# Kernel optimization log

Hardware: AMD Instinct MI355X
Metric: run time of the kernel (lower is better)

## Reference

```python
import jax, jax.numpy as jnp
import numpy as np

B, S, HID = 1, 4096, 2048
NH, NKV, HD = 16, 4, 128
BLK, LOCAL, GLOB, STRIDE = 128, 4, 4, 8
NEG = -1e9


def _rotate_half(x):
    x1 = x[..., : x.shape[-1] // 2]
    x2 = x[..., x.shape[-1] // 2 :]
    return jnp.concatenate([-x2, x1], axis=-1)


def setup_inputs() -> dict:
    key = jax.random.key(0)
    ks = jax.random.split(key, 6)
    hidden_states = jax.random.normal(ks[0], (B, S, HID), jnp.float32)
    attention_mask_2d = jnp.ones((B, S), jnp.float32)
    # RoPE tables (b=1 broadcasts over batch, heads)
    pos = jnp.arange(S, dtype=jnp.float32)
    inv = 1.0 / (10000.0 ** (jnp.arange(0, HD, 2, dtype=jnp.float32) / HD))
    fr = pos[:, None] * inv[None, :]
    emb = jnp.concatenate([fr, fr], axis=-1)
    cos = jnp.cos(emb)[None]
    sin = jnp.sin(emb)[None]
    sc = 0.02
    Wq = jax.random.normal(ks[1], (HID, NH * HD), jnp.float32) * sc
    Wk = jax.random.normal(ks[2], (HID, NKV * HD), jnp.float32) * sc
    Wv = jax.random.normal(ks[3], (HID, NKV * HD), jnp.float32) * sc
    Wo = jax.random.normal(ks[4], (NH * HD, HID), jnp.float32) * sc
    return dict(hidden_states=hidden_states, attention_mask_2d=attention_mask_2d,
                cos=cos, sin=sin, Wq=Wq, Wk=Wk, Wv=Wv, Wo=Wo)


def reference(hidden_states, attention_mask_2d, cos, sin, Wq, Wk, Wv, Wo):
    b, Sq, _ = hidden_states.shape
    q = (hidden_states @ Wq).reshape(b, Sq, NH, HD).transpose(0, 2, 1, 3)
    k = (hidden_states @ Wk).reshape(b, Sq, NKV, HD).transpose(0, 2, 1, 3)
    v = (hidden_states @ Wv).reshape(b, Sq, NKV, HD).transpose(0, 2, 1, 3)
    c, s = cos[:, None], sin[:, None]  # broadcast over heads
    q = q * c + _rotate_half(q) * s
    k = k * c + _rotate_half(k) * s
    rep = NH // NKV
    k = jnp.repeat(k, rep, axis=1)
    v = jnp.repeat(v, rep, axis=1)

    scaling = HD ** -0.5
    N = Sq // BLK  # seq divisible by block_size -> pad=0 in the original
    qb = q.reshape(b, NH, N, BLK, HD).astype(jnp.float32)
    kb = k.reshape(b, NH, N, BLK, HD).astype(jnp.float32)
    vb = v.reshape(b, NH, N, BLK, HD).astype(jnp.float32)
    km = attention_mask_2d.reshape(b, N, BLK)

    # ---- local windows: LOCAL blocks ending at the current block ----
    Lp = LOCAL - 1
    kp = jnp.pad(kb, ((0, 0), (0, 0), (Lp, 0), (0, 0), (0, 0)))
    vp = jnp.pad(vb, ((0, 0), (0, 0), (Lp, 0), (0, 0), (0, 0)))
    kmp = jnp.pad(km, ((0, 0), (Lp, 0), (0, 0)))  # padded blocks masked (0)
    win = jnp.arange(N)[:, None] + jnp.arange(LOCAL)[None, :]  # (N, LOCAL)
    k_local = kp[:, :, win]          # (b,h,N,LOCAL,BLK,HD)
    v_local = vp[:, :, win]
    km_local = kmp[:, win]           # (b,N,LOCAL,BLK)

    s_local = jnp.einsum('bhntd,bhnlsd->bhntls', qb, k_local) * scaling
    s_local = s_local + (1.0 - km_local)[:, None, :, None, :, :] * NEG
    intra = jnp.triu(jnp.full((BLK, BLK), NEG, jnp.float32), 1)  # causal inside current block only
    s_local = s_local.at[:, :, :, :, -1, :].add(intra)
    s_local = s_local.reshape(b, NH, N, BLK, LOCAL * BLK)

    # ---- global blocks: block 0 + strided past blocks, dedup -> masked ----
    i = jnp.arange(N)
    offsets = jnp.arange(GLOB - 1, 0, -1) * STRIDE
    idx = jnp.clip(i[:, None] - offsets[None, :], 0)
    idx = jnp.concatenate([jnp.zeros((N, 1), idx.dtype), idx], axis=1)  # (N, GLOB)
    dup = idx[:, 1:] == idx[:, :-1]
    g_valid = jnp.concatenate([jnp.ones((N, 1), bool), ~dup], axis=1).astype(jnp.float32)
    k_g = kb[:, :, idx]              # (b,h,N,GLOB,BLK,HD) gather of global blocks
    v_g = vb[:, :, idx]
    km_g = km[:, idx] * g_valid[None, :, :, None]  # (b,N,GLOB,BLK)

    s_g = jnp.einsum('bhntd,bhngsd->bhntgs', qb, k_g) * scaling
    s_g = s_g + (1.0 - km_g)[:, None, :, None, :, :] * NEG
    s_g = s_g.reshape(b, NH, N, BLK, GLOB * BLK)

    scores = jnp.concatenate([s_local, s_g], axis=-1)  # (b,h,N,BLK,(LOCAL+GLOB)*BLK)
    v_all = jnp.concatenate([v_local.reshape(b, NH, N, LOCAL * BLK, HD),
                             v_g.reshape(b, NH, N, GLOB * BLK, HD)], axis=-2)
    probs = jax.nn.softmax(scores, axis=-1)  # dropout_p = 0 (eval)
    out = jnp.einsum('bhntk,bhnkd->bhntd', probs, v_all)
    out = out.reshape(b, NH, Sq, HD).transpose(0, 2, 1, 3).reshape(b, Sq, NH * HD)
    return out @ Wo
```

## Files before the change

kernel.cpp:

```cpp
#include <hip/hip_runtime.h>
#include <hip/hip_bf16.h>
#include <cstdint>

#define NEGV   (-1000000000.0f)
#define SCALE  0.08838834764831845f
#define LOG2E  1.4426950408889634f
#define QSC    (SCALE * LOG2E)
#define NEGL2  (NEGV * LOG2E)

typedef __bf16 bf16x8 __attribute__((ext_vector_type(8)));
typedef float  f32x4  __attribute__((ext_vector_type(4)));
typedef unsigned short u16;
typedef unsigned int   u32;

#define MFMA16(a, b, c) __builtin_amdgcn_mfma_f32_16x16x32_bf16((a), (b), (c), 0, 0, 0)

#define WS_XP    ((size_t)0)
#define WS_AOP   ((size_t)0)
#define WS_WQP   ((size_t)8388608)
#define WS_WKP   ((size_t)12582912)
#define WS_WVP   ((size_t)13631488)
#define WS_WOP   ((size_t)14680064)
#define WS_QF    ((size_t)18874368)
#define WS_KF    ((size_t)27262976)
#define WS_VF    ((size_t)29360128)

__device__ __forceinline__ u16 f2bf(float f) {
  union { float f; u32 u; } v; v.f = f;
  u32 u = v.u;
  u += 0x7FFFu + ((u >> 16) & 1u);
  return (u16)(u >> 16);
}

__device__ __forceinline__ void gl_lds16(const u16* g, u16* l) {
  __builtin_amdgcn_global_load_lds((const __attribute__((address_space(1))) u32*)g,
                                   (__attribute__((address_space(3))) u32*)l,
                                   16, 0, 0);
}

__device__ __forceinline__ int fragoff(int row, int k) {
  return ((row >> 4) * 64 + ((k >> 3) & 3) * 16 + (row & 15)) * 8 + (k & 7);
}

__global__ __launch_bounds__(256, 4)
void convert_kernel(const float* __restrict__ X,
                    const float* __restrict__ Wq,
                    const float* __restrict__ Wk,
                    const float* __restrict__ Wv,
                    const float* __restrict__ Wo,
                    u16* __restrict__ ws)
{
  const int t = blockIdx.x;
  const int tid = threadIdx.x;
  const float* src; u16* dst; int tt, ldn; bool amode = false;
  if (t < 2048)      { src = X;  dst = ws + WS_XP;  tt = t;        ldn = 2048; amode = true; }
  else if (t < 3072) { src = Wq; dst = ws + WS_WQP; tt = t - 2048; ldn = 2048; }
  else if (t < 3328) { src = Wk; dst = ws + WS_WKP; tt = t - 3072; ldn = 512;  }
  else if (t < 3584) { src = Wv; dst = ws + WS_WVP; tt = t - 3328; ldn = 512;  }
  else               { src = Wo; dst = ws + WS_WOP; tt = t - 3584; ldn = 2048; }
  const int rb = tt >> 6, kb = tt & 63;

  if (amode) {
    #pragma unroll
    for (int p = 0; p < 2; ++p) {
      const int c = tid + 256 * p;
      const int row = (c >> 6) * 16 + (c & 15);
      const int k0  = ((c >> 4) & 3) * 8;
      union { u16 h[8]; uint4 v; } pk;
      const float* s0 = src + (size_t)(rb * 128 + row) * 2048 + kb * 32 + k0;
      const float4 a0 = *reinterpret_cast<const float4*>(s0);
      const float4 a1 = *reinterpret_cast<const float4*>(s0 + 4);
      pk.h[0] = f2bf(a0.x); pk.h[1] = f2bf(a0.y); pk.h[2] = f2bf(a0.z); pk.h[3] = f2bf(a0.w);
      pk.h[4] = f2bf(a1.x); pk.h[5] = f2bf(a1.y); pk.h[6] = f2bf(a1.z); pk.h[7] = f2bf(a1.w);
      *reinterpret_cast<uint4*>(dst + (size_t)tt * 4096 + c * 8) = pk.v;
    }
  } else {
    __shared__ u16 Ls[32][136];
    #pragma unroll
    for (int i = 0; i < 4; ++i) {
      const int c = tid + 256 * i;
      const int k = c >> 5, n4 = c & 31;
      const float4 wv = *reinterpret_cast<const float4*>(
          src + (size_t)(kb * 32 + k) * ldn + rb * 128 + n4 * 4);
      u16* d = &Ls[k][n4 * 4];
      d[0] = f2bf(wv.x); d[1] = f2bf(wv.y); d[2] = f2bf(wv.z); d[3] = f2bf(wv.w);
    }
    __syncthreads();
    #pragma unroll
    for (int p = 0; p < 2; ++p) {
      const int c = tid + 256 * p;
      const int row = (c >> 6) * 16 + (c & 15);
      const int k0  = ((c >> 4) & 3) * 8;
      union { u16 h[8]; uint4 v; } pk;
      #pragma unroll
      for (int j = 0; j < 8; ++j) pk.h[j] = Ls[k0 + j][row];
      *reinterpret_cast<uint4*>(dst + (size_t)tt * 4096 + c * 8) = pk.v;
    }
  }
}

__device__ __forceinline__ void gemm_core(const u16* __restrict__ pa,
                                          const u16* __restrict__ pb,
                                          u16* As, u16* Bs,
                                          int tid, int wave, int lane,
                                          f32x4 acc[2][8])
{
  for (int it = 0; it < 64; ++it) {
    __syncthreads();
    gl_lds16(pa + tid * 8,         As + tid * 8);
    gl_lds16(pa + (tid + 256) * 8, As + (tid + 256) * 8);
    gl_lds16(pb + tid * 8,         Bs + tid * 8);
    gl_lds16(pb + (tid + 256) * 8, Bs + (tid + 256) * 8);
    pa += 4096; pb += 4096;
    __syncthreads();
    bf16x8 af0 = *reinterpret_cast<const bf16x8*>(As + (wave * 2 + 0) * 512 + lane * 8);
    bf16x8 af1 = *reinterpret_cast<const bf16x8*>(As + (wave * 2 + 1) * 512 + lane * 8);
    #pragma unroll
    for (int nt = 0; nt < 8; ++nt) {
      const bf16x8 bfr = *reinterpret_cast<const bf16x8*>(Bs + nt * 512 + lane * 8);
      acc[0][nt] = MFMA16(af0, bfr, acc[0][nt]);
      acc[1][nt] = MFMA16(af1, bfr, acc[1][nt]);
    }
  }
}

__global__ __launch_bounds__(256, 2)
void qkv_kernel(const float* __restrict__ cosp,
                const float* __restrict__ sinp,
                u16* __restrict__ ws)
{
  const int mb = blockIdx.x, bn = blockIdx.y;
  const int tid = threadIdx.x;
  const int wave = tid >> 6, lane = tid & 63;
  const int lq = lane >> 4, l16 = lane & 15;

  const u16* Ab = ws + WS_XP + (size_t)mb * 64 * 4096;
  const u16* Bb; int seg, hh;
  if (bn < 16)      { Bb = ws + WS_WQP + (size_t)bn * 64 * 4096;        seg = 0; hh = bn; }
  else if (bn < 20) { Bb = ws + WS_WKP + (size_t)(bn - 16) * 64 * 4096; seg = 1; hh = bn - 16; }
  else              { Bb = ws + WS_WVP + (size_t)(bn - 20) * 64 * 4096; seg = 2; hh = bn - 20; }

  __shared__ __align__(16) u16 As[4096];
  __shared__ __align__(16) u16 Bs[4096];

  f32x4 acc[2][8];
  #pragma unroll
  for (int i = 0; i < 2; ++i)
    #pragma unroll
    for (int j = 0; j < 8; ++j)
      #pragma unroll
      for (int r = 0; r < 4; ++r) acc[i][j][r] = 0.0f;

  gemm_core(Ab, Bb, As, Bs, tid, wave, lane, acc);

  const int m0 = mb * 128;
  if (seg == 2) {
    u16* V = ws + WS_VF + (size_t)hh * 524288;
    #pragma unroll
    for (int mt = 0; mt < 2; ++mt)
      #pragma unroll
      for (int nt = 0; nt < 8; ++nt) {
        const int d = nt * 16 + l16;
        #pragma unroll
        for (int r = 0; r < 4; ++r) {
          const int s = m0 + wave * 32 + mt * 16 + lq * 4 + r;
          V[(s >> 5) * 4096 + fragoff(d, s & 31)] = f2bf(acc[mt][nt][r]);
        }
      }
  } else {
    u16* D = ws + ((seg == 0) ? WS_QF : WS_KF) + (size_t)hh * 524288;
    const float qs = (seg == 0) ? QSC : 1.0f;
    #pragma unroll
    for (int mt = 0; mt < 2; ++mt)
      #pragma unroll
      for (int r = 0; r < 4; ++r) {
        const int s = m0 + wave * 32 + mt * 16 + lq * 4 + r;
        const int sl = s & 127;
        u16* Dt = D + (size_t)(s >> 7) * 16384;
        #pragma unroll
        for (int nt = 0; nt < 4; ++nt) {
          const int d1 = nt * 16 + l16, d2 = d1 + 64;
          const float c  = cosp[s * 128 + d1];
          const float sn = sinp[s * 128 + d1];
          const float v1 = acc[mt][nt][r], v2 = acc[mt][nt + 4][r];
          Dt[(d1 >> 5) * 4096 + fragoff(sl, d1 & 31)] = f2bf((v1 * c - v2 * sn) * qs);
          Dt[(d2 >> 5) * 4096 + fragoff(sl, d2 & 31)] = f2bf((v2 * c + v1 * sn) * qs);
        }
      }
  }
}

__global__ __launch_bounds__(512, 2)
void attn_kernel(const float* __restrict__ amask, u16* __restrict__ ws)
{
  extern __shared__ u16 smem[];
  u16* bufK = smem;
  u16* bufV = smem + 16384;
  const int bx = blockIdx.x;
  const int n = 31 - (bx >> 4);
  const int h = bx & 15;
  const int kvh = h >> 2;
  const int tid = threadIdx.x;
  const int wave = tid >> 6, lane = tid & 63;
  const int lq = lane >> 4, l16 = lane & 15;

  const u16* Kfb = ws + WS_KF + (size_t)kvh * 524288;
  const u16* Vfb = ws + WS_VF + (size_t)kvh * 524288;
  u16* AOp = ws + WS_AOP;
  u16* Pw = smem + 32768 + wave * 2048;

  const u16* Qb = ws + WS_QF + (size_t)h * 524288 + (size_t)n * 16384;
  bf16x8 qf[4];
  #pragma unroll
  for (int kk = 0; kk < 4; ++kk)
    qf[kk] = *reinterpret_cast<const bf16x8*>(Qb + (size_t)kk * 4096 + (wave * 64 + lane) * 8);

  f32x4 O[8];
  #pragma unroll
  for (int j = 0; j < 8; ++j)
    #pragma unroll
    for (int r = 0; r < 4; ++r) O[j][r] = 0.0f;
  float mrow[4], lrow[4];
  #pragma unroll
  for (int r = 0; r < 4; ++r) { mrow[r] = -3.0e38f; lrow[r] = 0.0f; }

  const int L = (n < 3 ? n : 3) + 1;
  const int G = (n >= 25) ? 3 : (n >= 17) ? 2 : (n >= 9) ? 1 : 0;
  const int nv = L + 1 + G;
  #define KBOF(i) ((i) < L ? n - L + 1 + (i) : ((i) == L ? 0 : n - 8 * (G - ((i) - L - 1))))

  uint4 pk[4], pv[4]; float biasN[8];
  {
    const int b0 = KBOF(0);
    const u16* Kb = Kfb + (size_t)b0 * 16384;
    const u16* Vb = Vfb + (size_t)b0 * 16384;
    #pragma unroll
    for (int p = 0; p < 4; ++p) {
      pk[p] = *reinterpret_cast<const uint4*>(Kb + (tid + 512 * p) * 8);
      pv[p] = *reinterpret_cast<const uint4*>(Vb + (tid + 512 * p) * 8);
    }
    #pragma unroll
    for (int nt = 0; nt < 8; ++nt)
      biasN[nt] = (1.0f - amask[b0 * 128 + nt * 16 + l16]) * NEGL2;
  }

  #pragma unroll
  for (int i = 0; i < 8; ++i) {
    if (i >= nv) break;
    const bool intra = (i == L - 1);

    __syncthreads();
    #pragma unroll
    for (int p = 0; p < 4; ++p) {
      *reinterpret_cast<uint4*>(bufK + (tid + 512 * p) * 8) = pk[p];
      *reinterpret_cast<uint4*>(bufV + (tid + 512 * p) * 8) = pv[p];
    }
    float biasC[8];
    #pragma unroll
    for (int nt = 0; nt < 8; ++nt) biasC[nt] = biasN[nt];
    if (i + 1 < nv) {
      const int nb = KBOF(i + 1);
      const u16* Kb = Kfb + (size_t)nb * 16384;
      const u16* Vb = Vfb + (size_t)nb * 16384;
      #pragma unroll
      for (int p = 0; p < 4; ++p) {
        pk[p] = *reinterpret_cast<const uint4*>(Kb + (tid + 512 * p) * 8);
        pv[p] = *reinterpret_cast<const uint4*>(Vb + (tid + 512 * p) * 8);
      }
      #pragma unroll
      for (int nt = 0; nt < 8; ++nt)
        biasN[nt] = (1.0f - amask[nb * 128 + nt * 16 + l16]) * NEGL2;
    }
    __syncthreads();

    f32x4 sacc[8];
    #pragma unroll
    for (int j = 0; j < 8; ++j)
      #pragma unroll
      for (int r = 0; r < 4; ++r) sacc[j][r] = 0.0f;
    #pragma unroll
    for (int kk = 0; kk < 4; ++kk)
      #pragma unroll
      for (int nt = 0; nt < 8; ++nt) {
        const bf16x8 bfr = *reinterpret_cast<const bf16x8*>(
            bufK + ((kk * 8 + nt) * 64 + lane) * 8);
        sacc[nt] = MFMA16(qf[kk], bfr, sacc[nt]);
      }

    #pragma unroll
    for (int r = 0; r < 4; ++r) {
      const int tq = wave * 16 + lq * 4 + r;
      float sv[8];
      float rmax = -3.0e38f;
      #pragma unroll
      for (int nt = 0; nt < 8; ++nt) {
        float s = sacc[nt][r] + biasC[nt];
        const int tk = nt * 16 + l16;
        if (intra && tk > tq) s += NEGL2;
        sv[nt] = s;
        rmax = fmaxf(rmax, s);
      }
      #pragma unroll
      for (int off = 1; off < 16; off <<= 1)
        rmax = fmaxf(rmax, __shfl_xor(rmax, off, 64));
      const float mold = mrow[r];
      const float mnew = fmaxf(mold, rmax);
      const float alpha = exp2f(mold - mnew);
      float rsum = 0.0f;
      u16 pb[8];
      #pragma unroll
      for (int nt = 0; nt < 8; ++nt) {
        const float pe = exp2f(sv[nt] - mnew);
        rsum += pe;
        pb[nt] = f2bf(pe);
      }
      #pragma unroll
      for (int off = 1; off < 16; off <<= 1)
        rsum += __shfl_xor(rsum, off, 64);
      lrow[r] = lrow[r] * alpha + rsum;
      mrow[r] = mnew;
      #pragma unroll
      for (int nt = 0; nt < 8; ++nt) O[nt][r] *= alpha;
      #pragma unroll
      for (int nt = 0; nt < 8; ++nt)
        Pw[(nt >> 1) * 512 + ((((nt & 1) * 2 + (l16 >> 3)) * 16) + lq * 4 + r) * 8 + (l16 & 7)] = pb[nt];
    }

    #pragma unroll
    for (int kk = 0; kk < 4; ++kk) {
      const bf16x8 pf = *reinterpret_cast<const bf16x8*>(Pw + kk * 512 + lane * 8);
      #pragma unroll
      for (int nt = 0; nt < 8; ++nt) {
        const bf16x8 vfr = *reinterpret_cast<const bf16x8*>(
            bufV + ((kk * 8 + nt) * 64 + lane) * 8);
        O[nt] = MFMA16(pf, vfr, O[nt]);
      }
    }
  }
  #undef KBOF

  #pragma unroll
  for (int r = 0; r < 4; ++r) {
    const float inv = 1.0f / lrow[r];
    const int s = n * 128 + wave * 16 + lq * 4 + r;
    #pragma unroll
    for (int nt = 0; nt < 8; ++nt) {
      const int kcol = h * 128 + nt * 16 + l16;
      AOp[((size_t)(s >> 7) * 64 + (kcol >> 5)) * 4096 + fragoff(s & 127, kcol & 31)] =
          f2bf(O[nt][r] * inv);
    }
  }
}

__global__ __launch_bounds__(256, 2)
void outproj_kernel(const u16* __restrict__ ws, float* __restrict__ Out)
{
  const int mb = blockIdx.x, bn = blockIdx.y;
  const int tid = threadIdx.x;
  const int wave = tid >> 6, lane = tid & 63;
  const int lq = lane >> 4, l16 = lane & 15;

  const u16* Ab = ws + WS_AOP + (size_t)mb * 64 * 4096;
  const u16* Bb = ws + WS_WOP + (size_t)bn * 64 * 4096;

  __shared__ __align__(16) u16 As[4096];
  __shared__ __align__(16) u16 Bs[4096];

  f32x4 acc[2][8];
  #pragma unroll
  for (int i = 0; i < 2; ++i)
    #pragma unroll
    for (int j = 0; j < 8; ++j)
      #pragma unroll
      for (int r = 0; r < 4; ++r) acc[i][j][r] = 0.0f;

  gemm_core(Ab, Bb, (u16*)As, (u16*)Bs, tid, wave, lane, acc);

  #pragma unroll
  for (int mt = 0; mt < 2; ++mt)
    #pragma unroll
    for (int nt = 0; nt < 8; ++nt) {
      const int ccol = bn * 128 + nt * 16 + l16;
      #pragma unroll
      for (int r = 0; r < 4; ++r) {
        const int s = mb * 128 + wave * 32 + mt * 16 + lq * 4 + r;
        Out[(size_t)s * 2048 + ccol] = acc[mt][nt][r];
      }
    }
}

extern "C" void kernel_launch(void* const* d_in, const int* in_sizes, int n_in,
                              void* d_out, int out_size, void* d_ws, size_t ws_size,
                              hipStream_t stream) {
  const float* X     = (const float*)d_in[0];
  const float* amask = (const float*)d_in[1];
  const float* cosp  = (const float*)d_in[2];
  const float* sinp  = (const float*)d_in[3];
  const float* Wq    = (const float*)d_in[4];
  const float* Wk    = (const float*)d_in[5];
  const float* Wv    = (const float*)d_in[6];
  const float* Wo    = (const float*)d_in[7];
  float* Out = (float*)d_out;
  u16* ws = (u16*)d_ws;

  static int lds_set = 0;
  (void)hipFuncSetAttribute((const void*)attn_kernel,
                            hipFuncAttributeMaxDynamicSharedMemorySize, 98304);
  (void)lds_set;

  hipLaunchKernelGGL(convert_kernel, dim3(4608), dim3(256), 0, stream,
                     X, Wq, Wk, Wv, Wo, ws);
  hipLaunchKernelGGL(qkv_kernel, dim3(32, 24), dim3(256), 0, stream,
                     cosp, sinp, ws);
  hipLaunchKernelGGL(attn_kernel, dim3(512), dim3(512), 98304, stream,
                     amask, ws);
  hipLaunchKernelGGL(outproj_kernel, dim3(32, 16), dim3(256), 0, stream,
                     ws, Out);
}
```

Before: 345.5 us.

## Share K/V tiles across two heads per block with async double-buffered LDS loads

The attention kernel now has each 512-thread block handle two query heads of the same KV group, each wave covering 32 query rows, so every K/V tile staged in LDS serves twice as many MFMAs. Register-staged prefetch is replaced with direct global-to-LDS loads into a double buffer, removing a barrier per iteration and the register copy. The intent is to halve redundant K/V loads and overlap loading with compute. In exchange it uses 144KB of LDS and more registers per block, which limits occupancy, launches 256 blocks instead of 512, and drops the reversed block order that gave load balancing. Launch bounds for the two GEMM kernels are also raised to 3 blocks per CU.

```diff
diff --git a/kernel.cpp b/kernel.cpp
--- a/kernel.cpp
+++ b/kernel.cpp
@@ -124,7 +124,7 @@
   }
 }
 
-__global__ __launch_bounds__(256, 2)
+__global__ __launch_bounds__(256, 3)
 void qkv_kernel(const float* __restrict__ cosp,
                 const float* __restrict__ sinp,
                 u16* __restrict__ ws)
@@ -193,166 +193,180 @@
 __global__ __launch_bounds__(512, 2)
 void attn_kernel(const float* __restrict__ amask, u16* __restrict__ ws)
 {
-  extern __shared__ u16 smem[];
-  u16* bufK = smem;
-  u16* bufV = smem + 16384;
-  const int bx = blockIdx.x;
-  const int n = 31 - (bx >> 4);
-  const int h = bx & 15;
-  const int kvh = h >> 2;
+  extern __shared__ __align__(16) u16 smem[];
+  const int bx  = blockIdx.x;
+  const int n   = bx >> 3;
+  const int sub = bx & 7;
+  const int kvh = sub >> 1;
   const int tid = threadIdx.x;
   const int wave = tid >> 6, lane = tid & 63;
   const int lq = lane >> 4, l16 = lane & 15;
+  const int h = kvh * 4 + (sub & 1) * 2 + (wave >> 2);
+  const int wq = wave & 3;
 
   const u16* Kfb = ws + WS_KF + (size_t)kvh * 524288;
   const u16* Vfb = ws + WS_VF + (size_t)kvh * 524288;
   u16* AOp = ws + WS_AOP;
-  u16* Pw = smem + 32768 + wave * 2048;
+  u16* Pw = smem + 65536 + wave * 1024;
 
   const u16* Qb = ws + WS_QF + (size_t)h * 524288 + (size_t)n * 16384;
-  bf16x8 qf[4];
-  #pragma unroll
-  for (int kk = 0; kk < 4; ++kk)
-    qf[kk] = *reinterpret_cast<const bf16x8*>(Qb + (size_t)kk * 4096 + (wave * 64 + lane) * 8);
-
-  f32x4 O[8];
-  #pragma unroll
-  for (int j = 0; j < 8; ++j)
-    #pragma unroll
-    for (int r = 0; r < 4; ++r) O[j][r] = 0.0f;
-  float mrow[4], lrow[4];
-  #pragma unroll
-  for (int r = 0; r < 4; ++r) { mrow[r] = -3.0e38f; lrow[r] = 0.0f; }
+  bf16x8 qf[2][4];
+  #pragma unroll
+  for (int mt = 0; mt < 2; ++mt)
+    #pragma unroll
+    for (int kk = 0; kk < 4; ++kk)
+      qf[mt][kk] = *reinterpret_cast<const bf16x8*>(
+          Qb + (size_t)kk * 4096 + ((wq * 2 + mt) * 64 + lane) * 8);
+
+  f32x4 O[2][8];
+  #pragma unroll
+  for (int i = 0; i < 2; ++i)
+    #pragma unroll
+    for (int j = 0; j < 8; ++j)
+      #pragma unroll
+      for (int r = 0; r < 4; ++r) O[i][j][r] = 0.0f;
+  float mrow[2][4], lrow[2][4];
+  #pragma unroll
+  for (int i = 0; i < 2; ++i)
+    #pragma unroll
+    for (int r = 0; r < 4; ++r) { mrow[i][r] = -3.0e38f; lrow[i][r] = 0.0f; }
 
   const int L = (n < 3 ? n : 3) + 1;
   const int G = (n >= 25) ? 3 : (n >= 17) ? 2 : (n >= 9) ? 1 : 0;
   const int nv = L + 1 + G;
   #define KBOF(i) ((i) < L ? n - L + 1 + (i) : ((i) == L ? 0 : n - 8 * (G - ((i) - L - 1))))
 
-  uint4 pk[4], pv[4]; float biasN[8];
+  int nxt = KBOF(0);
   {
-    const int b0 = KBOF(0);
-    const u16* Kb = Kfb + (size_t)b0 * 16384;
-    const u16* Vb = Vfb + (size_t)b0 * 16384;
+    const u16* Kb = Kfb + (size_t)nxt * 16384;
+    const u16* Vb = Vfb + (size_t)nxt * 16384;
     #pragma unroll
     for (int p = 0; p < 4; ++p) {
-      pk[p] = *reinterpret_cast<const uint4*>(Kb + (tid + 512 * p) * 8);
-      pv[p] = *reinterpret_cast<const uint4*>(Vb + (tid + 512 * p) * 8);
-    }
+      gl_lds16(Kb + (tid + 512 * p) * 8, smem + (tid + 512 * p) * 8);
+      gl_lds16(Vb + (tid + 512 * p) * 8, smem + 16384 + (tid + 512 * p) * 8);
+    }
+  }
+
+  for (int i = 0; i < nv; ++i) {
+    const int cur = i & 1;
+    const int bcur = nxt;
+    const bool intra = (i == L - 1);
+    u16* bufK = smem + cur * 32768;
+    u16* bufV = bufK + 16384;
+
+    __syncthreads();
+
+    if (i + 1 < nv) {
+      nxt = KBOF(i + 1);
+      const u16* Kb = Kfb + (size_t)nxt * 16384;
+      const u16* Vb = Vfb + (size_t)nxt * 16384;
+      u16* dK = smem + (cur ^ 1) * 32768;
+      #pragma unroll
+      for (int p = 0; p < 4; ++p) {
+        gl_lds16(Kb + (tid + 512 * p) * 8, dK + (tid + 512 * p) * 8);
+        gl_lds16(Vb + (tid + 512 * p) * 8, dK + 16384 + (tid + 512 * p) * 8);
+      }
+    }
+
+    float bias[8];
     #pragma unroll
     for (int nt = 0; nt < 8; ++nt)
-      biasN[nt] = (1.0f - amask[b0 * 128 + nt * 16 + l16]) * NEGL2;
-  }
-
-  #pragma unroll
-  for (int i = 0; i < 8; ++i) {
-    if (i >= nv) break;
-    const bool intra = (i == L - 1);
-
-    __syncthreads();
-    #pragma unroll
-    for (int p = 0; p < 4; ++p) {
-      *reinterpret_cast<uint4*>(bufK + (tid + 512 * p) * 8) = pk[p];
-      *reinterpret_cast<uint4*>(bufV + (tid + 512 * p) * 8) = pv[p];
-    }
-    float biasC[8];
-    #pragma unroll
-    for (int nt = 0; nt < 8; ++nt) biasC[nt] = biasN[nt];
-    if (i + 1 < nv) {
-      const int nb = KBOF(i + 1);
-      const u16* Kb = Kfb + (size_t)nb * 16384;
-      const u16* Vb = Vfb + (size_t)nb * 16384;
-      #pragma unroll
-      for (int p = 0; p < 4; ++p) {
-        pk[p] = *reinterpret_cast<const uint4*>(Kb + (tid + 512 * p) * 8);
-        pv[p] = *reinterpret_cast<const uint4*>(Vb + (tid + 512 * p) * 8);
-      }
-      #pragma unroll
-      for (int nt = 0; nt < 8; ++nt)
-        biasN[nt] = (1.0f - amask[nb * 128 + nt * 16 + l16]) * NEGL2;
-    }
-    __syncthreads();
-
-    f32x4 sacc[8];
+      bias[nt] = (1.0f - amask[bcur * 128 + nt * 16 + l16]) * NEGL2;
+
+    f32x4 sacc[2][8];
     #pragma unroll
     for (int j = 0; j < 8; ++j)
       #pragma unroll
-      for (int r = 0; r < 4; ++r) sacc[j][r] = 0.0f;
+      for (int r = 0; r < 4; ++r) { sacc[0][j][r] = 0.0f; sacc[1][j][r] = 0.0f; }
     #pragma unroll
     for (int kk = 0; kk < 4; ++kk)
       #pragma unroll
       for (int nt = 0; nt < 8; ++nt) {
         const bf16x8 bfr = *reinterpret_cast<const bf16x8*>(
             bufK + ((kk * 8 + nt) * 64 + lane) * 8);
-        sacc[nt] = MFMA16(qf[kk], bfr, sacc[nt]);
-      }
-
-    #pragma unroll
-    for (int r = 0; r < 4; ++r) {
-      const int tq = wave * 16 + lq * 4 + r;
-      float sv[8];
-      float rmax = -3.0e38f;
-      #pragma unroll
-      for (int nt = 0; nt < 8; ++nt) {
-        float s = sacc[nt][r] + biasC[nt];
-        const int tk = nt * 16 + l16;
-        if (intra && tk > tq) s += NEGL2;
-        sv[nt] = s;
-        rmax = fmaxf(rmax, s);
-      }
-      #pragma unroll
-      for (int off = 1; off < 16; off <<= 1)
-        rmax = fmaxf(rmax, __shfl_xor(rmax, off, 64));
-      const float mold = mrow[r];
-      const float mnew = fmaxf(mold, rmax);
-      const float alpha = exp2f(mold - mnew);
-      float rsum = 0.0f;
-      u16 pb[8];
-      #pragma unroll
-      for (int nt = 0; nt < 8; ++nt) {
-        const float pe = exp2f(sv[nt] - mnew);
-        rsum += pe;
-        pb[nt] = f2bf(pe);
-      }
-      #pragma unroll
-      for (int off = 1; off < 16; off <<= 1)
-        rsum += __shfl_xor(rsum, off, 64);
-      lrow[r] = lrow[r] * alpha + rsum;
-      mrow[r] = mnew;
-      #pragma unroll
-      for (int nt = 0; nt < 8; ++nt) O[nt][r] *= alpha;
-      #pragma unroll
-      for (int nt = 0; nt < 8; ++nt)
-        Pw[(nt >> 1) * 512 + ((((nt & 1) * 2 + (l16 >> 3)) * 16) + lq * 4 + r) * 8 + (l16 & 7)] = pb[nt];
-    }
-
-    #pragma unroll
-    for (int kk = 0; kk < 4; ++kk) {
-      const bf16x8 pf = *reinterpret_cast<const bf16x8*>(Pw + kk * 512 + lane * 8);
+        sacc[0][nt] = MFMA16(qf[0][kk], bfr, sacc[0][nt]);
+        sacc[1][nt] = MFMA16(qf[1][kk], bfr, sacc[1][nt]);
+      }
+
+    u16 pbv[2][4][8];
+    #pragma unroll
+    for (int mt = 0; mt < 2; ++mt)
+      #pragma unroll
+      for (int r = 0; r < 4; ++r) {
+        const int tq = wq * 32 + mt * 16 + lq * 4 + r;
+        float sv[8];
+        float rmax = -3.0e38f;
+        #pragma unroll
+        for (int nt = 0; nt < 8; ++nt) {
+          float s = sacc[mt][nt][r] + bias[nt];
+          const int tk = nt * 16 + l16;
+          if (intra && tk > tq) s += NEGL2;
+          sv[nt] = s;
+          rmax = fmaxf(rmax, s);
+        }
+        #pragma unroll
+        for (int off = 1; off < 16; off <<= 1)
+          rmax = fmaxf(rmax, __shfl_xor(rmax, off, 64));
+        const float mold = mrow[mt][r];
+        const float mnew = fmaxf(mold, rmax);
+        const float alpha = exp2f(mold - mnew);
+        float rsum = 0.0f;
+        #pragma unroll
+        for (int nt = 0; nt < 8; ++nt) {
+          const float pe = exp2f(sv[nt] - mnew);
+          rsum += pe;
+          pbv[mt][r][nt] = f2bf(pe);
+        }
+        #pragma unroll
+        for (int off = 1; off < 16; off <<= 1)
+          rsum += __shfl_xor(rsum, off, 64);
+        lrow[mt][r] = lrow[mt][r] * alpha + rsum;
+        mrow[mt][r] = mnew;
+        #pragma unroll
+        for (int nt = 0; nt < 8; ++nt) O[mt][nt][r] *= alpha;
+      }
+
+    #pragma unroll
+    for (int c = 0; c < 4; ++c) {
+      #pragma unroll
+      for (int mt = 0; mt < 2; ++mt)
+        #pragma unroll
+        for (int r = 0; r < 4; ++r)
+          #pragma unroll
+          for (int j = 0; j < 2; ++j) {
+            const int nt = 2 * c + j;
+            Pw[mt * 512 + ((j * 2 + (l16 >> 3)) * 16 + lq * 4 + r) * 8 + (l16 & 7)] =
+                pbv[mt][r][nt];
+          }
+      const bf16x8 pf0 = *reinterpret_cast<const bf16x8*>(Pw + lane * 8);
+      const bf16x8 pf1 = *reinterpret_cast<const bf16x8*>(Pw + 512 + lane * 8);
       #pragma unroll
       for (int nt = 0; nt < 8; ++nt) {
         const bf16x8 vfr = *reinterpret_cast<const bf16x8*>(
-            bufV + ((kk * 8 + nt) * 64 + lane) * 8);
-        O[nt] = MFMA16(pf, vfr, O[nt]);
+            bufV + ((c * 8 + nt) * 64 + lane) * 8);
+        O[0][nt] = MFMA16(pf0, vfr, O[0][nt]);
+        O[1][nt] = MFMA16(pf1, vfr, O[1][nt]);
       }
     }
   }
   #undef KBOF
 
   #pragma unroll
-  for (int r = 0; r < 4; ++r) {
-    const float inv = 1.0f / lrow[r];
-    const int s = n * 128 + wave * 16 + lq * 4 + r;
-    #pragma unroll
-    for (int nt = 0; nt < 8; ++nt) {
-      const int kcol = h * 128 + nt * 16 + l16;
-      AOp[((size_t)(s >> 7) * 64 + (kcol >> 5)) * 4096 + fragoff(s & 127, kcol & 31)] =
-          f2bf(O[nt][r] * inv);
-    }
-  }
-}
-
-__global__ __launch_bounds__(256, 2)
+  for (int mt = 0; mt < 2; ++mt)
+    #pragma unroll
+    for (int r = 0; r < 4; ++r) {
+      const float inv = 1.0f / lrow[mt][r];
+      const int s = n * 128 + wq * 32 + mt * 16 + lq * 4 + r;
+      #pragma unroll
+      for (int nt = 0; nt < 8; ++nt) {
+        const int kcol = h * 128 + nt * 16 + l16;
+        AOp[((size_t)(s >> 7) * 64 + (kcol >> 5)) * 4096 + fragoff(s & 127, kcol & 31)] =
+            f2bf(O[mt][nt][r] * inv);
+      }
+    }
+}
+
+__global__ __launch_bounds__(256, 3)
 void outproj_kernel(const u16* __restrict__ ws, float* __restrict__ Out)
 {
   const int mb = blockIdx.x, bn = blockIdx.y;
@@ -403,16 +417,14 @@
   float* Out = (float*)d_out;
   u16* ws = (u16*)d_ws;
 
-  static int lds_set = 0;
   (void)hipFuncSetAttribute((const void*)attn_kernel,
-                            hipFuncAttributeMaxDynamicSharedMemorySize, 98304);
-  (void)lds_set;
+                            hipFuncAttributeMaxDynamicSharedMemorySize, 147456);
 
   hipLaunchKernelGGL(convert_kernel, dim3(4608), dim3(256), 0, stream,
                      X, Wq, Wk, Wv, Wo, ws);
   hipLaunchKernelGGL(qkv_kernel, dim3(32, 24), dim3(256), 0, stream,
                      cosp, sinp, ws);
-  hipLaunchKernelGGL(attn_kernel, dim3(512), dim3(512), 98304, stream,
+  hipLaunchKernelGGL(attn_kernel, dim3(256), dim3(512), 147456, stream,
                      amask, ws);
   hipLaunchKernelGGL(outproj_kernel, dim3(32, 16), dim3(256), 0, stream,
                      ws, Out);
```

Measured after the change: 298.6 us. -13.6%, faster.
